# Optimization experiments

Measured on AMD Instinct MI355X. Metric: run time of the kernel, lower is better.

Reference implementation:

```python
import jax, jax.numpy as jnp
import numpy as np

B, S, E, HEADS, LATENT = 8, 4096, 2048, 16, 64
HEAD_SIZE = E // HEADS  # 128
NEG = -1e20


def setup_inputs() -> dict:
    key = jax.random.key(0)
    k0, k1, k2, k3, k4 = jax.random.split(key, 5)
    return {
        "x": jax.random.normal(k0, (B, S, E), dtype=jnp.float32) * 0.02,
        "W_dkv": jax.random.normal(k1, (LATENT, E), dtype=jnp.float32) * 0.02,
        "W_k": jax.random.normal(k2, (HEAD_SIZE, LATENT), dtype=jnp.float32) * 0.02,
        "W_v": jax.random.normal(k3, (HEAD_SIZE, LATENT), dtype=jnp.float32) * 0.02,
        "W_q": jax.random.normal(k4, (HEAD_SIZE, E), dtype=jnp.float32) * 0.02,
    }


def reference(x, W_dkv, W_k, W_v, W_q):
    # x: [B,S,E]; nn.Linear computes x @ W.T (weight layout [out,in])
    head_size = W_k.shape[0]
    latent = jnp.einsum("bse,le->bsl", x, W_dkv)        # latent KV cache [B,S,L]
    absorbed_q = W_q.T @ W_k                              # [E,H] @ [H,L] -> [E,L]
    q_res = jnp.einsum("bse,el->bsl", x, absorbed_q)     # [B,S,L]
    scale = head_size ** -0.5
    scores = jnp.einsum("bql,bkl->bqk", q_res, latent) * scale  # [B,S,S]
    seq = x.shape[1]
    causal = jnp.tril(jnp.ones((seq, seq), dtype=bool))
    scores = jnp.where(causal, scores, NEG)
    attn = jax.nn.softmax(scores, axis=-1)               # dropout skipped (eval mode)
    v = jnp.einsum("bsl,hl->bsh", latent, W_v)           # compressed V [B,S,H]
    out = jnp.einsum("bqk,bkh->bqh", attn, v)            # [B,S,head_size]
    return out, latent  # latent == kv_cache returned by the module
```

## Files before the change

### kernel.cpp

```cpp
#include <hip/hip_runtime.h>
#include <hip/hip_bf16.h>

#define NB 8
#define NS 4096
#define NE 2048
#define NL 64
#define NH 128
#define NM (NB*NS)
#define NQT (NS/64)

typedef unsigned short ushort_t;
typedef __attribute__((ext_vector_type(4))) float f32x4;
typedef __attribute__((ext_vector_type(8))) __bf16 bf16x8;
typedef __attribute__((ext_vector_type(8))) unsigned short u16x8;
typedef __attribute__((ext_vector_type(4))) unsigned short u16x4;

#define SCALE2 0.1275174537f

__device__ __forceinline__ float fast_exp2(float x) {
    return __builtin_amdgcn_exp2f(x);
}

__device__ __forceinline__ unsigned short f2bf(float f) {
    union { float f; unsigned u; } v; v.f = f;
    unsigned u = v.u + 0x7fffu + ((v.u >> 16) & 1u);
    return (unsigned short)(u >> 16);
}

__device__ __forceinline__ int swz(int row, int colbyte) {
    return (row * 128 + colbyte) ^ ((row & 7) << 4);
}

__device__ __forceinline__ void wg_barrier() {
    asm volatile("s_waitcnt lgkmcnt(0)" ::: "memory");
    __builtin_amdgcn_s_barrier();
    __builtin_amdgcn_sched_barrier(0);
}

__global__ __launch_bounds__(256) void prep_kernel(
    const float* __restrict__ Wdkv, const float* __restrict__ Wk,
    const float* __restrict__ Wq, ushort_t* __restrict__ WcatT)
{
    __shared__ float wk[128 * 64];
    const int t = threadIdx.x;
    for (int i = t; i < 128 * 64; i += 256) wk[i] = Wk[i];
    __syncthreads();
    const int e = blockIdx.x * 256 + t;
    const int l0 = blockIdx.y * 16;
    float acc[16];
    #pragma unroll
    for (int l = 0; l < 16; ++l) acc[l] = 0.f;
    for (int h = 0; h < 128; ++h) {
        float q = Wq[h * NE + e];
        #pragma unroll
        for (int l = 0; l < 16; ++l) acc[l] += q * wk[h * 64 + l0 + l];
    }
    for (int l = 0; l < 16; ++l) WcatT[(64 + l0 + l) * NE + e] = f2bf(acc[l] * SCALE2);
    for (int l = 0; l < 16; ++l) WcatT[(l0 + l) * NE + e] = f2bf(Wdkv[(l0 + l) * NE + e]);
}

__global__ __launch_bounds__(256) void proj_kernel(
    const float* __restrict__ x, const ushort_t* __restrict__ WcatT,
    float* __restrict__ latent_out, ushort_t* __restrict__ k_bf,
    ushort_t* __restrict__ q_bf, ushort_t* __restrict__ kt)
{
    __shared__ ushort_t As[2][64 * 64];
    __shared__ ushort_t Bs[2][128 * 64];
    const int tid = threadIdx.x;
    const int w = tid >> 6, lane = tid & 63, lg = lane >> 4, li = lane & 15;
    const int m0 = blockIdx.x * 64;
    const int wm = (w >> 1) * 32, wn = (w & 1) * 64;
    const int srow = tid >> 3, scol = tid & 7;

    f32x4 acc[2][4];
    #pragma unroll
    for (int i = 0; i < 2; ++i)
        #pragma unroll
        for (int j = 0; j < 4; ++j) acc[i][j] = f32x4{0.f, 0.f, 0.f, 0.f};

    f32x4 a0reg[2][2], a1reg[2][2];
    u16x8 b0reg[4], b1reg[4];

#define PLOAD(k0, AR, BR) do { \
    _Pragma("unroll") for (int p = 0; p < 2; ++p) { \
        const float* gp = x + (long)(m0 + srow + 32 * p) * NE + (k0) + scol * 8; \
        AR[p][0] = *reinterpret_cast<const f32x4*>(gp); \
        AR[p][1] = *reinterpret_cast<const f32x4*>(gp + 4); } \
    _Pragma("unroll") for (int p = 0; p < 4; ++p) \
        BR[p] = *reinterpret_cast<const u16x8*>(WcatT + (long)(srow + 32 * p) * NE + (k0) + scol * 8); \
} while (0)

#define PWRITE(AR, BR, buf) do { \
    _Pragma("unroll") for (int p = 0; p < 2; ++p) { \
        u16x8 h; \
        _Pragma("unroll") for (int j = 0; j < 4; ++j) { h[j] = f2bf(AR[p][0][j]); h[4 + j] = f2bf(AR[p][1][j]); } \
        *reinterpret_cast<u16x8*>(reinterpret_cast<char*>(As[buf]) + swz(srow + 32 * p, scol * 16)) = h; } \
    _Pragma("unroll") for (int p = 0; p < 4; ++p) \
        *reinterpret_cast<u16x8*>(reinterpret_cast<char*>(Bs[buf]) + swz(srow + 32 * p, scol * 16)) = BR[p]; \
} while (0)

    auto compute = [&](int buf) {
        #pragma unroll
        for (int c = 0; c < 2; ++c) {
            bf16x8 af[2], bfv[4];
            #pragma unroll
            for (int mf = 0; mf < 2; ++mf)
                af[mf] = *reinterpret_cast<const bf16x8*>(
                    reinterpret_cast<const char*>(As[buf]) + swz(wm + 16 * mf + li, c * 64 + lg * 16));
            #pragma unroll
            for (int nf = 0; nf < 4; ++nf)
                bfv[nf] = *reinterpret_cast<const bf16x8*>(
                    reinterpret_cast<const char*>(Bs[buf]) + swz(wn + 16 * nf + li, c * 64 + lg * 16));
            #pragma unroll
            for (int mf = 0; mf < 2; ++mf)
                #pragma unroll
                for (int nf = 0; nf < 4; ++nf)
                    acc[mf][nf] = __builtin_amdgcn_mfma_f32_16x16x32_bf16(
                        af[mf], bfv[nf], acc[mf][nf], 0, 0, 0);
        }
    };

    PLOAD(0, a0reg, b0reg);
    PLOAD(64, a1reg, b1reg);
    PWRITE(a0reg, b0reg, 0);
    wg_barrier();

    for (int ks = 0; ks < 32; ks += 2) {
        if (ks + 2 < 32) PLOAD((ks + 2) * 64, a0reg, b0reg);
        compute(0);
        PWRITE(a1reg, b1reg, 1);
        wg_barrier();
        if (ks + 3 < 32) PLOAD((ks + 3) * 64, a1reg, b1reg);
        compute(1);
        if (ks + 2 < 32) PWRITE(a0reg, b0reg, 0);
        wg_barrier();
    }

    const int b = m0 >> 12, s0 = m0 & 4095;
    #pragma unroll
    for (int mf = 0; mf < 2; ++mf) {
        #pragma unroll
        for (int nf = 0; nf < 4; ++nf) {
            int col = wn + 16 * nf + li;
            #pragma unroll
            for (int r = 0; r < 4; ++r) {
                int row = m0 + wm + 16 * mf + 4 * lg + r;
                float v = acc[mf][nf][r];
                if (wn == 0) {
                    latent_out[(long)row * NL + col] = v;
                    k_bf[(long)row * NL + col] = f2bf(v);
                    *reinterpret_cast<ushort_t*>(reinterpret_cast<char*>(As[0]) +
                        swz(wm + 16 * mf + 4 * lg + r, col * 2)) = f2bf(v);
                } else {
                    q_bf[(long)row * NL + (col - 64)] = f2bf(v);
                }
            }
        }
    }
    wg_barrier();
    union { u16x8 u; bf16x8 v; } iu;
    #pragma unroll
    for (int j = 0; j < 8; ++j)
        iu.u[j] = (lg == (li >> 3) + 2 * (w & 1) && (li & 7) == j)
                      ? (ushort_t)0x3F80 : (ushort_t)0;
    const int ckt = w >> 1;
    f32x4 ktacc[4];
    #pragma unroll
    for (int nf = 0; nf < 4; ++nf) {
        bf16x8 bfv = *reinterpret_cast<const bf16x8*>(
            reinterpret_cast<const char*>(As[0]) + swz(16 * nf + li, ckt * 64 + lg * 16));
        ktacc[nf] = __builtin_amdgcn_mfma_f32_16x16x32_bf16(
            iu.v, bfv, f32x4{0.f, 0.f, 0.f, 0.f}, 0, 0, 0);
    }
    #pragma unroll
    for (int nf = 0; nf < 4; ++nf)
        #pragma unroll
        for (int r = 0; r < 4; ++r)
            kt[(long)(b * 64 + 16 * w + 4 * lg + r) * NS + s0 + 16 * nf + li] =
                f2bf(ktacc[nf][r]);
}

__global__ __launch_bounds__(256) void attn_kernel(
    const ushort_t* __restrict__ q_bf, const ushort_t* __restrict__ k_bf,
    const ushort_t* __restrict__ kt, float* __restrict__ Opart,
    float* __restrict__ lpart, float* __restrict__ mpart)
{
    __shared__ ushort_t Ks[2][64 * 64];
    __shared__ ushort_t KTs[2][64 * 64];
    const int tid = threadIdx.x;
    const int w = tid >> 6, lane = tid & 63, lg = lane >> 4, li = lane & 15;
    const int l = blockIdx.x;
    const int b = l & 7;
    const int j = l >> 3;
    const int h = j >> 6;
    const int p_ = j & 63;
    const int k_ = p_ >> 1, e_ = p_ & 1, kk = (k_ & 15) * 2;
    const int qt = (k_ >> 4) ? (e_ ? kk + 1 : 63 - kk) : (e_ ? 62 - kk : kk);
    const int niter = (qt + 2 - h) >> 1;
    const bool hasdiag = ((qt - h) & 1) == 0;
    const int Q0 = qt << 6;
    const int srow = tid >> 3, scol = tid & 7;
    const int vc0 = 64 * ((scol >> 1) & 1) + 32 * (scol & 1) + 8 * (scol >> 2);

    const long qrow = (long)b * NS + Q0 + 16 * w + li;
    bf16x8 qf[2];
    qf[0] = *reinterpret_cast<const bf16x8*>(q_bf + qrow * NL + 0 + lg * 8);
    qf[1] = *reinterpret_cast<const bf16x8*>(q_bf + qrow * NL + 32 + lg * 8);

    float m_r = -3.0e38f, l_r = 0.f;
    f32x4 oacc[4];
    #pragma unroll
    for (int n = 0; n < 4; ++n) oacc[n] = f32x4{0.f, 0.f, 0.f, 0.f};

    u16x8 k0reg[2], t0reg[2], k1reg[2], t1reg[2];

#define ALOAD(kv0, KR, TR) do { \
    _Pragma("unroll") for (int p = 0; p < 2; ++p) \
        KR[p] = *reinterpret_cast<const u16x8*>(k_bf + ((long)b * NS + (kv0) + srow + 32 * p) * NL + scol * 8); \
    _Pragma("unroll") for (int p = 0; p < 2; ++p) \
        TR[p] = *reinterpret_cast<const u16x8*>(kt + (long)(b * 64 + srow + 32 * p) * NS + (kv0) + scol * 8); \
} while (0)

#define AWRITE(KR, TR, buf) do { \
    _Pragma("unroll") for (int p = 0; p < 2; ++p) \
        *reinterpret_cast<u16x8*>(reinterpret_cast<char*>(Ks[buf]) + swz(srow + 32 * p, scol * 16)) = KR[p]; \
    _Pragma("unroll") for (int p = 0; p < 2; ++p) { \
        u16x4 lo = {TR[p][0], TR[p][1], TR[p][2], TR[p][3]}; \
        u16x4 hi = {TR[p][4], TR[p][5], TR[p][6], TR[p][7]}; \
        *reinterpret_cast<u16x4*>(reinterpret_cast<char*>(KTs[buf]) + swz(srow + 32 * p, vc0)) = lo; \
        *reinterpret_cast<u16x4*>(reinterpret_cast<char*>(KTs[buf]) + swz(srow + 32 * p, vc0 + 16)) = hi; \
    } \
} while (0)

    auto compute = [&](int buf, bool diag) {
        const char* Kb = reinterpret_cast<const char*>(Ks[buf]);
        const char* Tb = reinterpret_cast<const char*>(KTs[buf]);
        f32x4 s[4];
        #pragma unroll
        for (int f = 0; f < 4; ++f) s[f] = f32x4{0.f, 0.f, 0.f, 0.f};
        __builtin_amdgcn_s_setprio(1);
        #pragma unroll
        for (int c = 0; c < 2; ++c)
            #pragma unroll
            for (int f = 0; f < 4; ++f) {
                bf16x8 a = *reinterpret_cast<const bf16x8*>(Kb + swz(16 * f + li, c * 64 + lg * 16));
                s[f] = __builtin_amdgcn_mfma_f32_16x16x32_bf16(a, qf[c], s[f], 0, 0, 0);
            }
        __builtin_amdgcn_s_setprio(0);
        float p[16];
        float mx = -3.0e38f;
        #pragma unroll
        for (int f = 0; f < 4; ++f)
            #pragma unroll
            for (int r = 0; r < 4; ++r) {
                float v = s[f][r];
                if (diag && (16 * f + 4 * lg + r) > (16 * w + li)) v = -3.0e38f;
                p[f * 4 + r] = v;
                mx = fmaxf(mx, v);
            }
        if (!__all(mx <= m_r + 8.f)) {
            float mxf = fmaxf(mx, __shfl_xor(mx, 16));
            mxf = fmaxf(mxf, __shfl_xor(mxf, 32));
            float m_new = fmaxf(m_r, mxf);
            float corr = fast_exp2(m_r - m_new);
            m_r = m_new;
            l_r *= corr;
            float corrO[4];
            #pragma unroll
            for (int r = 0; r < 4; ++r)
                corrO[r] = __shfl(corr, (lane & 48) | (4 * lg + r));
            #pragma unroll
            for (int n = 0; n < 4; ++n)
                #pragma unroll
                for (int r = 0; r < 4; ++r) oacc[n][r] *= corrO[r];
        }
        float rs = 0.f;
        #pragma unroll
        for (int i = 0; i < 16; ++i) { p[i] = fast_exp2(p[i] - m_r); rs += p[i]; }
        l_r += rs;
        unsigned pw[8];
        #pragma unroll
        for (int f = 0; f < 4; ++f)
            #pragma unroll
            for (int hh = 0; hh < 2; ++hh)
                asm("v_cvt_pk_bf16_f32 %0, %1, %2"
                    : "=v"(pw[2 * f + hh]) : "v"(p[4 * f + 2 * hh]), "v"(p[4 * f + 2 * hh + 1]));
        union { unsigned u[4]; bf16x8 v; } pa0, pa1;
        pa0.u[0] = pw[0]; pa0.u[1] = pw[1]; pa0.u[2] = pw[4]; pa0.u[3] = pw[5];
        pa1.u[0] = pw[2]; pa1.u[1] = pw[3]; pa1.u[2] = pw[6]; pa1.u[3] = pw[7];
        __builtin_amdgcn_s_setprio(1);
        #pragma unroll
        for (int c = 0; c < 2; ++c) {
            bf16x8 pa = c ? pa1.v : pa0.v;
            #pragma unroll
            for (int n = 0; n < 4; ++n) {
                bf16x8 vb = *reinterpret_cast<const bf16x8*>(Tb + swz(16 * n + li, c * 64 + lg * 16));
                oacc[n] = __builtin_amdgcn_mfma_f32_16x16x32_bf16(pa, vb, oacc[n], 0, 0, 0);
            }
        }
        __builtin_amdgcn_s_setprio(0);
    };

    if (niter > 0) {
        ALOAD(h * 64, k0reg, t0reg);
        if (niter >= 2) ALOAD((h + 2) * 64, k1reg, t1reg);
        AWRITE(k0reg, t0reg, 0);
        wg_barrier();
        for (int i = 0; i < niter; i += 2) {
            if (i + 2 < niter) ALOAD((h + 2 * (i + 2)) * 64, k0reg, t0reg);
            compute(0, hasdiag && (i == niter - 1));
            if (i + 1 < niter) AWRITE(k1reg, t1reg, 1);
            wg_barrier();
            if (i + 1 >= niter) break;
            if (i + 3 < niter) ALOAD((h + 2 * (i + 3)) * 64, k1reg, t1reg);
            compute(1, hasdiag && (i + 1 == niter - 1));
            if (i + 2 < niter) AWRITE(k0reg, t0reg, 0);
            wg_barrier();
        }
    }

    l_r += __shfl_xor(l_r, 16);
    l_r += __shfl_xor(l_r, 32);
    const int IB = ((h * NB + b) << 6) + qt;
    if (lane < 16)  {
        lpart[IB * 64 + 16 * w + li] = l_r;
        mpart[IB * 64 + 16 * w + li] = m_r;
    }
    #pragma unroll
    for (int n = 0; n < 4; ++n)
        #pragma unroll
        for (int r = 0; r < 4; ++r)
            Opart[((long)IB * 64 + 16 * w + 4 * lg + r) * NL + 16 * n + li] = oacc[n][r];
}

__global__ __launch_bounds__(256) void merge_kernel(
    const float* __restrict__ Opart, const float* __restrict__ lpart,
    const float* __restrict__ mpart, const float* __restrict__ Wv,
    float* __restrict__ out)
{
    __shared__ ushort_t Ms[64 * 64];
    __shared__ ushort_t Wvs[128 * 64];
    __shared__ float Os[64 * 132];
    const int blk = blockIdx.x;
    const int b = blk >> 6, qt = blk & 63;
    const int tid = threadIdx.x;
    const int w = tid >> 6, lane = tid & 63, lg = lane >> 4, li = lane & 15;

    {
        const int r = tid >> 1, hf = tid & 1;
        const float* wp = Wv + r * 64 + hf * 32;
        #pragma unroll
        for (int q = 0; q < 2; ++q) {
            f32x4 w0 = *reinterpret_cast<const f32x4*>(wp + q * 16);
            f32x4 w1 = *reinterpret_cast<const f32x4*>(wp + q * 16 + 4);
            f32x4 w2 = *reinterpret_cast<const f32x4*>(wp + q * 16 + 8);
            f32x4 w3 = *reinterpret_cast<const f32x4*>(wp + q * 16 + 12);
            u16x8 h0, h1;
            #pragma unroll
            for (int jj = 0; jj < 4; ++jj) {
                h0[jj] = f2bf(w0[jj]); h0[4 + jj] = f2bf(w1[jj]);
                h1[jj] = f2bf(w2[jj]); h1[4 + jj] = f2bf(w3[jj]);
            }
            *reinterpret_cast<u16x8*>(reinterpret_cast<char*>(Wvs) + swz(r, hf * 64 + q * 32)) = h0;
            *reinterpret_cast<u16x8*>(reinterpret_cast<char*>(Wvs) + swz(r, hf * 64 + q * 32 + 16)) = h1;
        }
    }
    {
        const int r = tid >> 2, c0 = (tid & 3) * 16;
        const long L1 = ((long)((b << 6) + qt)) * 64 + r;
        const long L2 = ((long)(((NB + b) << 6) + qt)) * 64 + r;
        float l1 = lpart[L1], m1 = mpart[L1];
        float l2 = lpart[L2], m2 = mpart[L2];
        float M = fmaxf(m1, m2);
        float w1 = fast_exp2(m1 - M), w2 = fast_exp2(m2 - M);
        float inv = 1.f / (w1 * l1 + w2 * l2);
        float a1 = w1 * inv, a2 = w2 * inv;
        const float* o1 = Opart + L1 * NL;
        const float* o2 = Opart + L2 * NL;
        #pragma unroll
        for (int q = 0; q < 4; ++q) {
            int col = c0 + q * 4;
            f32x4 A = *reinterpret_cast<const f32x4*>(o1 + col);
            f32x4 Bv = *reinterpret_cast<const f32x4*>(o2 + col);
            u16x4 hh;
            #pragma unroll
            for (int k = 0; k < 4; ++k) hh[k] = f2bf(A[k] * a1 + Bv[k] * a2);
            *reinterpret_cast<u16x4*>(reinterpret_cast<char*>(Ms) + swz(r, col * 2)) = hh;
        }
    }
    __syncthreads();
    f32x4 vacc[2][4];
    #pragma unroll
    for (int i = 0; i < 2; ++i)
        #pragma unroll
        for (int jj = 0; jj < 4; ++jj) vacc[i][jj] = f32x4{0.f, 0.f, 0.f, 0.f};
    #pragma unroll
    for (int c = 0; c < 2; ++c) {
        bf16x8 af[2], bfv[4];
        #pragma unroll
        for (int mf = 0; mf < 2; ++mf)
            af[mf] = *reinterpret_cast<const bf16x8*>(
                reinterpret_cast<const char*>(Wvs) + swz(32 * w + 16 * mf + li, c * 64 + lg * 16));
        #pragma unroll
        for (int nf = 0; nf < 4; ++nf)
            bfv[nf] = *reinterpret_cast<const bf16x8*>(
                reinterpret_cast<const char*>(Ms) + swz(16 * nf + li, c * 64 + lg * 16));
        #pragma unroll
        for (int mf = 0; mf < 2; ++mf)
            #pragma unroll
            for (int nf = 0; nf < 4; ++nf)
                vacc[mf][nf] = __builtin_amdgcn_mfma_f32_16x16x32_bf16(
                    af[mf], bfv[nf], vacc[mf][nf], 0, 0, 0);
    }
    #pragma unroll
    for (int mf = 0; mf < 2; ++mf)
        #pragma unroll
        for (int nf = 0; nf < 4; ++nf)
            #pragma unroll
            for (int r = 0; r < 4; ++r)
                Os[(16 * nf + li) * 132 + 32 * w + 16 * mf + 4 * lg + r] = vacc[mf][nf][r];
    __syncthreads();
    {
        const int r = tid >> 2, cb = (tid & 3) * 32;
        float* op = out + ((long)b * NS + qt * 64 + r) * NH + cb;
        const float* sp = Os + r * 132 + cb;
        #pragma unroll
        for (int q = 0; q < 8; ++q)
            *reinterpret_cast<f32x4*>(op + 4 * q) = *reinterpret_cast<const f32x4*>(sp + 4 * q);
    }
}

extern "C" void kernel_launch(void* const* d_in, const int* in_sizes, int n_in,
                              void* d_out, int out_size, void* d_ws, size_t ws_size,
                              hipStream_t stream) {
    const float* x    = (const float*)d_in[0];
    const float* Wdkv = (const float*)d_in[1];
    const float* Wk   = (const float*)d_in[2];
    const float* Wv   = (const float*)d_in[3];
    const float* Wq   = (const float*)d_in[4];

    float* out = (float*)d_out;
    float* latent_out = out + (long)NM * NH;

    ushort_t* WcatT = (ushort_t*)d_ws;
    ushort_t* q_bf  = WcatT + 128 * NE;
    ushort_t* k_bf  = q_bf + (long)NM * NL;
    ushort_t* kt    = k_bf + (long)NM * NL;
    float* Opart = (float*)(kt + (long)NM * NL);
    float* lpart = Opart + (long)2 * NB * NQT * 64 * NL;
    float* mpart = lpart + 2 * NB * NQT * 64;

    hipLaunchKernelGGL(prep_kernel, dim3(NE / 256, 4), dim3(256), 0, stream, Wdkv, Wk, Wq, WcatT);
    hipLaunchKernelGGL(proj_kernel, dim3(NM / 64), dim3(256), 0, stream,
                       x, WcatT, latent_out, k_bf, q_bf, kt);
    hipLaunchKernelGGL(attn_kernel, dim3(1024), dim3(256), 0, stream,
                       q_bf, k_bf, kt, Opart, lpart, mpart);
    hipLaunchKernelGGL(merge_kernel, dim3(NB * NQT), dim3(256), 0, stream,
                       Opart, lpart, mpart, Wv, out);
}
```

Measured before the change: 142.8 us.

## Fuse attention and merge into one kernel with intra-block split-KV reduction

Removes the separate merge kernel and the global Opart/lpart/mpart partials. Each attention block now owns a 64-query tile. Its four waves each process a 32-key slice of every 128-key chunk for all four 16-query sub-blocks. The per-wave partial outputs are merged through LDS and the Wv projection runs in the same kernel. The grid halves to 512 blocks with 64KB of LDS and launch_bounds(256,2), which trades a kernel launch and global round-trip for fewer blocks, higher register pressure and a bf16 intermediate in the merge. The proj kernel's fp32-to-bf16 conversion also switches to the packed v_cvt_pk_bf16_f32 instruction.

```diff
diff --git a/kernel.cpp b/kernel.cpp
--- a/kernel.cpp
+++ b/kernel.cpp
@@ -7,7 +7,6 @@
 #define NL 64
 #define NH 128
 #define NM (NB*NS)
-#define NQT (NS/64)
 
 typedef unsigned short ushort_t;
 typedef __attribute__((ext_vector_type(4))) float f32x4;
@@ -25,6 +24,10 @@
     union { float f; unsigned u; } v; v.f = f;
     unsigned u = v.u + 0x7fffu + ((v.u >> 16) & 1u);
     return (unsigned short)(u >> 16);
+}
+
+__device__ __forceinline__ float bf2f(ushort_t u) {
+    union { unsigned u; float f; } v; v.u = (unsigned)u << 16; return v.f;
 }
 
 __device__ __forceinline__ int swz(int row, int colbyte) {
@@ -92,9 +95,12 @@
 
 #define PWRITE(AR, BR, buf) do { \
     _Pragma("unroll") for (int p = 0; p < 2; ++p) { \
-        u16x8 h; \
-        _Pragma("unroll") for (int j = 0; j < 4; ++j) { h[j] = f2bf(AR[p][0][j]); h[4 + j] = f2bf(AR[p][1][j]); } \
-        *reinterpret_cast<u16x8*>(reinterpret_cast<char*>(As[buf]) + swz(srow + 32 * p, scol * 16)) = h; } \
+        union { unsigned uw[4]; u16x8 v; } hu; \
+        asm("v_cvt_pk_bf16_f32 %0, %1, %2" : "=v"(hu.uw[0]) : "v"(AR[p][0][0]), "v"(AR[p][0][1])); \
+        asm("v_cvt_pk_bf16_f32 %0, %1, %2" : "=v"(hu.uw[1]) : "v"(AR[p][0][2]), "v"(AR[p][0][3])); \
+        asm("v_cvt_pk_bf16_f32 %0, %1, %2" : "=v"(hu.uw[2]) : "v"(AR[p][1][0]), "v"(AR[p][1][1])); \
+        asm("v_cvt_pk_bf16_f32 %0, %1, %2" : "=v"(hu.uw[3]) : "v"(AR[p][1][2]), "v"(AR[p][1][3])); \
+        *reinterpret_cast<u16x8*>(reinterpret_cast<char*>(As[buf]) + swz(srow + 32 * p, scol * 16)) = hu.v; } \
     _Pragma("unroll") for (int p = 0; p < 4; ++p) \
         *reinterpret_cast<u16x8*>(reinterpret_cast<char*>(Bs[buf]) + swz(srow + 32 * p, scol * 16)) = BR[p]; \
 } while (0)
@@ -180,220 +186,262 @@
                 f2bf(ktacc[nf][r]);
 }
 
-__global__ __launch_bounds__(256) void attn_kernel(
+__global__ __launch_bounds__(256, 2) void attn_kernel(
     const ushort_t* __restrict__ q_bf, const ushort_t* __restrict__ k_bf,
-    const ushort_t* __restrict__ kt, float* __restrict__ Opart,
-    float* __restrict__ lpart, float* __restrict__ mpart)
+    const ushort_t* __restrict__ kt, const float* __restrict__ Wv,
+    float* __restrict__ out)
 {
-    __shared__ ushort_t Ks[2][64 * 64];
-    __shared__ ushort_t KTs[2][64 * 64];
+    __shared__ __attribute__((aligned(16))) char smem[65536];
+    ushort_t* OW = (ushort_t*)smem;
+    float* mw = (float*)(smem + 32768);
+    float* lw = (float*)(smem + 33792);
+    ushort_t* Ms = (ushort_t*)(smem + 36864);
+    ushort_t* Wvs = (ushort_t*)(smem + 45056);
+    float* Os = (float*)smem;
+
     const int tid = threadIdx.x;
     const int w = tid >> 6, lane = tid & 63, lg = lane >> 4, li = lane & 15;
     const int l = blockIdx.x;
     const int b = l & 7;
-    const int j = l >> 3;
-    const int h = j >> 6;
-    const int p_ = j & 63;
+    const int p_ = l >> 3;
     const int k_ = p_ >> 1, e_ = p_ & 1, kk = (k_ & 15) * 2;
     const int qt = (k_ >> 4) ? (e_ ? kk + 1 : 63 - kk) : (e_ ? 62 - kk : kk);
-    const int niter = (qt + 2 - h) >> 1;
-    const bool hasdiag = ((qt - h) & 1) == 0;
     const int Q0 = qt << 6;
-    const int srow = tid >> 3, scol = tid & 7;
-    const int vc0 = 64 * ((scol >> 1) & 1) + 32 * (scol & 1) + 8 * (scol >> 2);
-
-    const long qrow = (long)b * NS + Q0 + 16 * w + li;
-    bf16x8 qf[2];
-    qf[0] = *reinterpret_cast<const bf16x8*>(q_bf + qrow * NL + 0 + lg * 8);
-    qf[1] = *reinterpret_cast<const bf16x8*>(q_bf + qrow * NL + 32 + lg * 8);
-
-    float m_r = -3.0e38f, l_r = 0.f;
-    f32x4 oacc[4];
-    #pragma unroll
-    for (int n = 0; n < 4; ++n) oacc[n] = f32x4{0.f, 0.f, 0.f, 0.f};
-
-    u16x8 k0reg[2], t0reg[2], k1reg[2], t1reg[2];
-
-#define ALOAD(kv0, KR, TR) do { \
-    _Pragma("unroll") for (int p = 0; p < 2; ++p) \
-        KR[p] = *reinterpret_cast<const u16x8*>(k_bf + ((long)b * NS + (kv0) + srow + 32 * p) * NL + scol * 8); \
-    _Pragma("unroll") for (int p = 0; p < 2; ++p) \
-        TR[p] = *reinterpret_cast<const u16x8*>(kt + (long)(b * 64 + srow + 32 * p) * NS + (kv0) + scol * 8); \
+    const int nch = (qt >> 1) + 1;
+
+    const int krow = tid >> 1, khalf = tid & 1;
+    const int trow = tid >> 2, tkq = (tid & 3) * 32;
+
+    bf16x8 qf[4][2];
+    #pragma unroll
+    for (int qb = 0; qb < 4; ++qb)
+        #pragma unroll
+        for (int c = 0; c < 2; ++c)
+            qf[qb][c] = *reinterpret_cast<const bf16x8*>(
+                q_bf + ((long)b * NS + Q0 + 16 * qb + li) * NL + c * 32 + lg * 8);
+
+    float m_r[4], l_r[4];
+    #pragma unroll
+    for (int qb = 0; qb < 4; ++qb) { m_r[qb] = -1.0e30f; l_r[qb] = 0.f; }
+    f32x4 oacc[4][4];
+    #pragma unroll
+    for (int qb = 0; qb < 4; ++qb)
+        #pragma unroll
+        for (int n = 0; n < 4; ++n) oacc[qb][n] = f32x4{0.f, 0.f, 0.f, 0.f};
+
+    u16x8 k0reg[4], t0reg[4], k1reg[4], t1reg[4];
+
+#define ALOAD(ch, KR, TR) do { \
+    const int kv0_ = (ch) * 128; \
+    _Pragma("unroll") for (int pp = 0; pp < 4; ++pp) \
+        KR[pp] = *reinterpret_cast<const u16x8*>( \
+            k_bf + ((long)b * NS + kv0_ + krow) * NL + khalf * 32 + pp * 8); \
+    _Pragma("unroll") for (int pp = 0; pp < 4; ++pp) \
+        TR[pp] = *reinterpret_cast<const u16x8*>( \
+            kt + ((long)b * 64 + trow) * NS + kv0_ + tkq + pp * 8); \
 } while (0)
 
 #define AWRITE(KR, TR, buf) do { \
-    _Pragma("unroll") for (int p = 0; p < 2; ++p) \
-        *reinterpret_cast<u16x8*>(reinterpret_cast<char*>(Ks[buf]) + swz(srow + 32 * p, scol * 16)) = KR[p]; \
-    _Pragma("unroll") for (int p = 0; p < 2; ++p) { \
-        u16x4 lo = {TR[p][0], TR[p][1], TR[p][2], TR[p][3]}; \
-        u16x4 hi = {TR[p][4], TR[p][5], TR[p][6], TR[p][7]}; \
-        *reinterpret_cast<u16x4*>(reinterpret_cast<char*>(KTs[buf]) + swz(srow + 32 * p, vc0)) = lo; \
-        *reinterpret_cast<u16x4*>(reinterpret_cast<char*>(KTs[buf]) + swz(srow + 32 * p, vc0 + 16)) = hi; \
+    char* Kb_ = smem + (buf) * 16384; \
+    char* Tb_ = smem + 32768 + (buf) * 16384; \
+    _Pragma("unroll") for (int pp = 0; pp < 4; ++pp) \
+        *reinterpret_cast<u16x8*>(Kb_ + swz(krow, khalf * 64 + pp * 16)) = KR[pp]; \
+    _Pragma("unroll") for (int pp = 0; pp < 4; ++pp) { \
+        const int kv8 = tkq + pp * 8; \
+        const int colp = (kv8 & 0x60) | ((kv8 & 0xC) << 1) | ((kv8 & 0x10) >> 2); \
+        const int xo = (trow & 15) << 4; \
+        u16x4 lo = {TR[pp][0], TR[pp][1], TR[pp][2], TR[pp][3]}; \
+        u16x4 hi = {TR[pp][4], TR[pp][5], TR[pp][6], TR[pp][7]}; \
+        *reinterpret_cast<u16x4*>(Tb_ + trow * 256 + ((colp * 2) ^ xo)) = lo; \
+        *reinterpret_cast<u16x4*>(Tb_ + trow * 256 + (((colp + 8) * 2) ^ xo)) = hi; \
     } \
 } while (0)
 
-    auto compute = [&](int buf, bool diag) {
-        const char* Kb = reinterpret_cast<const char*>(Ks[buf]);
-        const char* Tb = reinterpret_cast<const char*>(KTs[buf]);
-        f32x4 s[4];
-        #pragma unroll
-        for (int f = 0; f < 4; ++f) s[f] = f32x4{0.f, 0.f, 0.f, 0.f};
+    auto compute = [&](int buf, bool diag, int kv0) {
+        const char* Kb = smem + buf * 16384;
+        const char* Tb = smem + 32768 + buf * 16384;
+        f32x4 s[2][4];
+        #pragma unroll
+        for (int kvb = 0; kvb < 2; ++kvb)
+            #pragma unroll
+            for (int qb = 0; qb < 4; ++qb) s[kvb][qb] = f32x4{0.f, 0.f, 0.f, 0.f};
         __builtin_amdgcn_s_setprio(1);
         #pragma unroll
         for (int c = 0; c < 2; ++c)
             #pragma unroll
-            for (int f = 0; f < 4; ++f) {
-                bf16x8 a = *reinterpret_cast<const bf16x8*>(Kb + swz(16 * f + li, c * 64 + lg * 16));
-                s[f] = __builtin_amdgcn_mfma_f32_16x16x32_bf16(a, qf[c], s[f], 0, 0, 0);
+            for (int kvb = 0; kvb < 2; ++kvb) {
+                bf16x8 a = *reinterpret_cast<const bf16x8*>(
+                    Kb + swz(32 * w + 16 * kvb + li, c * 64 + lg * 16));
+                #pragma unroll
+                for (int qb = 0; qb < 4; ++qb)
+                    s[kvb][qb] = __builtin_amdgcn_mfma_f32_16x16x32_bf16(
+                        a, qf[qb][c], s[kvb][qb], 0, 0, 0);
             }
         __builtin_amdgcn_s_setprio(0);
-        float p[16];
-        float mx = -3.0e38f;
-        #pragma unroll
-        for (int f = 0; f < 4; ++f)
-            #pragma unroll
-            for (int r = 0; r < 4; ++r) {
-                float v = s[f][r];
-                if (diag && (16 * f + 4 * lg + r) > (16 * w + li)) v = -3.0e38f;
-                p[f * 4 + r] = v;
-                mx = fmaxf(mx, v);
+        if (diag) {
+            #pragma unroll
+            for (int kvb = 0; kvb < 2; ++kvb)
+                #pragma unroll
+                for (int qb = 0; qb < 4; ++qb)
+                    #pragma unroll
+                    for (int r = 0; r < 4; ++r) {
+                        int kv_g = kv0 + 32 * w + 16 * kvb + 4 * lg + r;
+                        int q_g = Q0 + 16 * qb + li;
+                        if (kv_g > q_g) s[kvb][qb][r] = -3.0e38f;
+                    }
+        }
+        float mx[4];
+        #pragma unroll
+        for (int qb = 0; qb < 4; ++qb) {
+            float m0_ = fmaxf(fmaxf(s[0][qb][0], s[0][qb][1]), fmaxf(s[0][qb][2], s[0][qb][3]));
+            float m1_ = fmaxf(fmaxf(s[1][qb][0], s[1][qb][1]), fmaxf(s[1][qb][2], s[1][qb][3]));
+            mx[qb] = fmaxf(m0_, m1_);
+        }
+        bool ok = (mx[0] <= m_r[0] + 8.f) && (mx[1] <= m_r[1] + 8.f) &&
+                  (mx[2] <= m_r[2] + 8.f) && (mx[3] <= m_r[3] + 8.f);
+        if (!__all(ok)) {
+            #pragma unroll
+            for (int qb = 0; qb < 4; ++qb) {
+                float mxf = fmaxf(mx[qb], __shfl_xor(mx[qb], 16));
+                mxf = fmaxf(mxf, __shfl_xor(mxf, 32));
+                float m_new = fmaxf(m_r[qb], mxf);
+                float corr = fast_exp2(m_r[qb] - m_new);
+                m_r[qb] = m_new;
+                l_r[qb] *= corr;
+                float corrO[4];
+                #pragma unroll
+                for (int r = 0; r < 4; ++r)
+                    corrO[r] = __shfl(corr, (lane & 48) | (4 * lg + r));
+                #pragma unroll
+                for (int n = 0; n < 4; ++n)
+                    #pragma unroll
+                    for (int r = 0; r < 4; ++r) oacc[qb][n][r] *= corrO[r];
             }
-        if (!__all(mx <= m_r + 8.f)) {
-            float mxf = fmaxf(mx, __shfl_xor(mx, 16));
-            mxf = fmaxf(mxf, __shfl_xor(mxf, 32));
-            float m_new = fmaxf(m_r, mxf);
-            float corr = fast_exp2(m_r - m_new);
-            m_r = m_new;
-            l_r *= corr;
-            float corrO[4];
-            #pragma unroll
-            for (int r = 0; r < 4; ++r)
-                corrO[r] = __shfl(corr, (lane & 48) | (4 * lg + r));
+        }
+        #pragma unroll
+        for (int qb = 0; qb < 4; ++qb) {
+            float rs = 0.f;
+            #pragma unroll
+            for (int kvb = 0; kvb < 2; ++kvb)
+                #pragma unroll
+                for (int r = 0; r < 4; ++r) {
+                    float pv = fast_exp2(s[kvb][qb][r] - m_r[qb]);
+                    s[kvb][qb][r] = pv;
+                    rs += pv;
+                }
+            l_r[qb] += rs;
+        }
+        bf16x8 vb[4];
+        #pragma unroll
+        for (int n = 0; n < 4; ++n)
+            vb[n] = *reinterpret_cast<const bf16x8*>(
+                Tb + (16 * n + li) * 256 + ((64 * w + 16 * lg) ^ (li << 4)));
+        __builtin_amdgcn_s_setprio(1);
+        #pragma unroll
+        for (int qb = 0; qb < 4; ++qb) {
+            union { unsigned uw[4]; bf16x8 v; } pa;
+            asm("v_cvt_pk_bf16_f32 %0, %1, %2" : "=v"(pa.uw[0]) : "v"(s[0][qb][0]), "v"(s[0][qb][1]));
+            asm("v_cvt_pk_bf16_f32 %0, %1, %2" : "=v"(pa.uw[1]) : "v"(s[0][qb][2]), "v"(s[0][qb][3]));
+            asm("v_cvt_pk_bf16_f32 %0, %1, %2" : "=v"(pa.uw[2]) : "v"(s[1][qb][0]), "v"(s[1][qb][1]));
+            asm("v_cvt_pk_bf16_f32 %0, %1, %2" : "=v"(pa.uw[3]) : "v"(s[1][qb][2]), "v"(s[1][qb][3]));
             #pragma unroll
             for (int n = 0; n < 4; ++n)
-                #pragma unroll
-                for (int r = 0; r < 4; ++r) oacc[n][r] *= corrO[r];
-        }
-        float rs = 0.f;
-        #pragma unroll
-        for (int i = 0; i < 16; ++i) { p[i] = fast_exp2(p[i] - m_r); rs += p[i]; }
-        l_r += rs;
-        unsigned pw[8];
-        #pragma unroll
-        for (int f = 0; f < 4; ++f)
-            #pragma unroll
-            for (int hh = 0; hh < 2; ++hh)
-                asm("v_cvt_pk_bf16_f32 %0, %1, %2"
-                    : "=v"(pw[2 * f + hh]) : "v"(p[4 * f + 2 * hh]), "v"(p[4 * f + 2 * hh + 1]));
-        union { unsigned u[4]; bf16x8 v; } pa0, pa1;
-        pa0.u[0] = pw[0]; pa0.u[1] = pw[1]; pa0.u[2] = pw[4]; pa0.u[3] = pw[5];
-        pa1.u[0] = pw[2]; pa1.u[1] = pw[3]; pa1.u[2] = pw[6]; pa1.u[3] = pw[7];
-        __builtin_amdgcn_s_setprio(1);
-        #pragma unroll
-        for (int c = 0; c < 2; ++c) {
-            bf16x8 pa = c ? pa1.v : pa0.v;
-            #pragma unroll
-            for (int n = 0; n < 4; ++n) {
-                bf16x8 vb = *reinterpret_cast<const bf16x8*>(Tb + swz(16 * n + li, c * 64 + lg * 16));
-                oacc[n] = __builtin_amdgcn_mfma_f32_16x16x32_bf16(pa, vb, oacc[n], 0, 0, 0);
-            }
+                oacc[qb][n] = __builtin_amdgcn_mfma_f32_16x16x32_bf16(
+                    pa.v, vb[n], oacc[qb][n], 0, 0, 0);
         }
         __builtin_amdgcn_s_setprio(0);
     };
 
-    if (niter > 0) {
-        ALOAD(h * 64, k0reg, t0reg);
-        if (niter >= 2) ALOAD((h + 2) * 64, k1reg, t1reg);
-        AWRITE(k0reg, t0reg, 0);
+    ALOAD(0, k0reg, t0reg);
+    if (nch >= 2) ALOAD(1, k1reg, t1reg);
+    AWRITE(k0reg, t0reg, 0);
+    wg_barrier();
+    for (int i = 0; i < nch; i += 2) {
+        if (i + 2 < nch) ALOAD(i + 2, k0reg, t0reg);
+        compute(0, i == nch - 1, i * 128);
+        if (i + 1 < nch) AWRITE(k1reg, t1reg, 1);
         wg_barrier();
-        for (int i = 0; i < niter; i += 2) {
-            if (i + 2 < niter) ALOAD((h + 2 * (i + 2)) * 64, k0reg, t0reg);
-            compute(0, hasdiag && (i == niter - 1));
-            if (i + 1 < niter) AWRITE(k1reg, t1reg, 1);
-            wg_barrier();
-            if (i + 1 >= niter) break;
-            if (i + 3 < niter) ALOAD((h + 2 * (i + 3)) * 64, k1reg, t1reg);
-            compute(1, hasdiag && (i + 1 == niter - 1));
-            if (i + 2 < niter) AWRITE(k0reg, t0reg, 0);
-            wg_barrier();
-        }
-    }
-
-    l_r += __shfl_xor(l_r, 16);
-    l_r += __shfl_xor(l_r, 32);
-    const int IB = ((h * NB + b) << 6) + qt;
-    if (lane < 16)  {
-        lpart[IB * 64 + 16 * w + li] = l_r;
-        mpart[IB * 64 + 16 * w + li] = m_r;
-    }
-    #pragma unroll
-    for (int n = 0; n < 4; ++n)
-        #pragma unroll
-        for (int r = 0; r < 4; ++r)
-            Opart[((long)IB * 64 + 16 * w + 4 * lg + r) * NL + 16 * n + li] = oacc[n][r];
-}
-
-__global__ __launch_bounds__(256) void merge_kernel(
-    const float* __restrict__ Opart, const float* __restrict__ lpart,
-    const float* __restrict__ mpart, const float* __restrict__ Wv,
-    float* __restrict__ out)
-{
-    __shared__ ushort_t Ms[64 * 64];
-    __shared__ ushort_t Wvs[128 * 64];
-    __shared__ float Os[64 * 132];
-    const int blk = blockIdx.x;
-    const int b = blk >> 6, qt = blk & 63;
-    const int tid = threadIdx.x;
-    const int w = tid >> 6, lane = tid & 63, lg = lane >> 4, li = lane & 15;
+        if (i + 1 >= nch) break;
+        if (i + 3 < nch) ALOAD(i + 3, k1reg, t1reg);
+        compute(1, i + 1 == nch - 1, (i + 1) * 128);
+        if (i + 2 < nch) AWRITE(k0reg, t0reg, 0);
+        wg_barrier();
+    }
+
+    #pragma unroll
+    for (int qb = 0; qb < 4; ++qb) {
+        l_r[qb] += __shfl_xor(l_r[qb], 16);
+        l_r[qb] += __shfl_xor(l_r[qb], 32);
+    }
+    if (lg == 0) {
+        #pragma unroll
+        for (int qb = 0; qb < 4; ++qb) {
+            mw[w * 64 + 16 * qb + li] = m_r[qb];
+            lw[w * 64 + 16 * qb + li] = l_r[qb];
+        }
+    }
+    #pragma unroll
+    for (int qb = 0; qb < 4; ++qb)
+        #pragma unroll
+        for (int r = 0; r < 4; ++r) {
+            union { unsigned uw[2]; u16x4 v; } u;
+            asm("v_cvt_pk_bf16_f32 %0, %1, %2" : "=v"(u.uw[0]) : "v"(oacc[qb][0][r]), "v"(oacc[qb][1][r]));
+            asm("v_cvt_pk_bf16_f32 %0, %1, %2" : "=v"(u.uw[1]) : "v"(oacc[qb][2][r]), "v"(oacc[qb][3][r]));
+            int q = 16 * qb + 4 * lg + r;
+            *reinterpret_cast<u16x4*>(OW + (w * 64 + q) * 64 + li * 4) = u.v;
+        }
+    wg_barrier();
 
     {
+        const int q = tid >> 2, g = tid & 3;
+        float m4[4], l4[4];
+        #pragma unroll
+        for (int ww = 0; ww < 4; ++ww) { m4[ww] = mw[ww * 64 + q]; l4[ww] = lw[ww * 64 + q]; }
+        float M = fmaxf(fmaxf(m4[0], m4[1]), fmaxf(m4[2], m4[3]));
+        float cw[4], L = 0.f;
+        #pragma unroll
+        for (int ww = 0; ww < 4; ++ww) { cw[ww] = fast_exp2(m4[ww] - M); L += cw[ww] * l4[ww]; }
+        float inv = 1.f / L;
+        float merged[16];
+        #pragma unroll
+        for (int e = 0; e < 16; ++e) {
+            float a = 0.f;
+            #pragma unroll
+            for (int ww = 0; ww < 4; ++ww)
+                a += cw[ww] * bf2f(OW[(ww * 64 + q) * 64 + e * 4 + g]);
+            merged[e] = a * inv;
+        }
+        #pragma unroll
+        for (int ee = 0; ee < 8; ++ee) {
+            unsigned pk;
+            asm("v_cvt_pk_bf16_f32 %0, %1, %2" : "=v"(pk) : "v"(merged[2 * ee]), "v"(merged[2 * ee + 1]));
+            *reinterpret_cast<unsigned*>(reinterpret_cast<char*>(Ms) + swz(q, g * 32 + 4 * ee)) = pk;
+        }
         const int r = tid >> 1, hf = tid & 1;
         const float* wp = Wv + r * 64 + hf * 32;
         #pragma unroll
-        for (int q = 0; q < 2; ++q) {
-            f32x4 w0 = *reinterpret_cast<const f32x4*>(wp + q * 16);
-            f32x4 w1 = *reinterpret_cast<const f32x4*>(wp + q * 16 + 4);
-            f32x4 w2 = *reinterpret_cast<const f32x4*>(wp + q * 16 + 8);
-            f32x4 w3 = *reinterpret_cast<const f32x4*>(wp + q * 16 + 12);
+        for (int qq = 0; qq < 2; ++qq) {
+            f32x4 w0 = *reinterpret_cast<const f32x4*>(wp + qq * 16);
+            f32x4 w1 = *reinterpret_cast<const f32x4*>(wp + qq * 16 + 4);
+            f32x4 w2 = *reinterpret_cast<const f32x4*>(wp + qq * 16 + 8);
+            f32x4 w3 = *reinterpret_cast<const f32x4*>(wp + qq * 16 + 12);
             u16x8 h0, h1;
             #pragma unroll
             for (int jj = 0; jj < 4; ++jj) {
                 h0[jj] = f2bf(w0[jj]); h0[4 + jj] = f2bf(w1[jj]);
                 h1[jj] = f2bf(w2[jj]); h1[4 + jj] = f2bf(w3[jj]);
             }
-            *reinterpret_cast<u16x8*>(reinterpret_cast<char*>(Wvs) + swz(r, hf * 64 + q * 32)) = h0;
-            *reinterpret_cast<u16x8*>(reinterpret_cast<char*>(Wvs) + swz(r, hf * 64 + q * 32 + 16)) = h1;
-        }
-    }
-    {
-        const int r = tid >> 2, c0 = (tid & 3) * 16;
-        const long L1 = ((long)((b << 6) + qt)) * 64 + r;
-        const long L2 = ((long)(((NB + b) << 6) + qt)) * 64 + r;
-        float l1 = lpart[L1], m1 = mpart[L1];
-        float l2 = lpart[L2], m2 = mpart[L2];
-        float M = fmaxf(m1, m2);
-        float w1 = fast_exp2(m1 - M), w2 = fast_exp2(m2 - M);
-        float inv = 1.f / (w1 * l1 + w2 * l2);
-        float a1 = w1 * inv, a2 = w2 * inv;
-        const float* o1 = Opart + L1 * NL;
-        const float* o2 = Opart + L2 * NL;
-        #pragma unroll
-        for (int q = 0; q < 4; ++q) {
-            int col = c0 + q * 4;
-            f32x4 A = *reinterpret_cast<const f32x4*>(o1 + col);
-            f32x4 Bv = *reinterpret_cast<const f32x4*>(o2 + col);
-            u16x4 hh;
-            #pragma unroll
-            for (int k = 0; k < 4; ++k) hh[k] = f2bf(A[k] * a1 + Bv[k] * a2);
-            *reinterpret_cast<u16x4*>(reinterpret_cast<char*>(Ms) + swz(r, col * 2)) = hh;
-        }
-    }
-    __syncthreads();
+            *reinterpret_cast<u16x8*>(reinterpret_cast<char*>(Wvs) + swz(r, hf * 64 + qq * 32)) = h0;
+            *reinterpret_cast<u16x8*>(reinterpret_cast<char*>(Wvs) + swz(r, hf * 64 + qq * 32 + 16)) = h1;
+        }
+    }
+    wg_barrier();
+
     f32x4 vacc[2][4];
     #pragma unroll
     for (int i = 0; i < 2; ++i)
         #pragma unroll
-        for (int jj = 0; jj < 4; ++jj) vacc[i][jj] = f32x4{0.f, 0.f, 0.f, 0.f};
+        for (int j = 0; j < 4; ++j) vacc[i][j] = f32x4{0.f, 0.f, 0.f, 0.f};
     #pragma unroll
     for (int c = 0; c < 2; ++c) {
         bf16x8 af[2], bfv[4];
@@ -412,6 +460,7 @@
                 vacc[mf][nf] = __builtin_amdgcn_mfma_f32_16x16x32_bf16(
                     af[mf], bfv[nf], vacc[mf][nf], 0, 0, 0);
     }
+    wg_barrier();
     #pragma unroll
     for (int mf = 0; mf < 2; ++mf)
         #pragma unroll
@@ -419,14 +468,14 @@
             #pragma unroll
             for (int r = 0; r < 4; ++r)
                 Os[(16 * nf + li) * 132 + 32 * w + 16 * mf + 4 * lg + r] = vacc[mf][nf][r];
-    __syncthreads();
+    wg_barrier();
     {
         const int r = tid >> 2, cb = (tid & 3) * 32;
-        float* op = out + ((long)b * NS + qt * 64 + r) * NH + cb;
+        float* op = out + ((long)b * NS + Q0 + r) * NH + cb;
         const float* sp = Os + r * 132 + cb;
         #pragma unroll
-        for (int q = 0; q < 8; ++q)
-            *reinterpret_cast<f32x4*>(op + 4 * q) = *reinterpret_cast<const f32x4*>(sp + 4 * q);
+        for (int qq = 0; qq < 8; ++qq)
+            *reinterpret_cast<f32x4*>(op + 4 * qq) = *reinterpret_cast<const f32x4*>(sp + 4 * qq);
     }
 }
 
@@ -446,15 +495,10 @@
     ushort_t* q_bf  = WcatT + 128 * NE;
     ushort_t* k_bf  = q_bf + (long)NM * NL;
     ushort_t* kt    = k_bf + (long)NM * NL;
-    float* Opart = (float*)(kt + (long)NM * NL);
-    float* lpart = Opart + (long)2 * NB * NQT * 64 * NL;
-    float* mpart = lpart + 2 * NB * NQT * 64;
 
     hipLaunchKernelGGL(prep_kernel, dim3(NE / 256, 4), dim3(256), 0, stream, Wdkv, Wk, Wq, WcatT);
     hipLaunchKernelGGL(proj_kernel, dim3(NM / 64), dim3(256), 0, stream,
                        x, WcatT, latent_out, k_bf, q_bf, kt);
-    hipLaunchKernelGGL(attn_kernel, dim3(1024), dim3(256), 0, stream,
-                       q_bf, k_bf, kt, Opart, lpart, mpart);
-    hipLaunchKernelGGL(merge_kernel, dim3(NB * NQT), dim3(256), 0, stream,
-                       Opart, lpart, mpart, Wv, out);
-}
+    hipLaunchKernelGGL(attn_kernel, dim3(512), dim3(256), 0, stream,
+                       q_bf, k_bf, kt, Wv, out);
+}
```

Result: faster. 133.4 us (median of 2 runs) (-6.6%).
